# Performance work log

Hardware: AMD Instinct MI355X
Metric: run time of the kernel (lower is better)

The kernel has to match this reference:

```python
import jax, jax.numpy as jnp
import numpy as np

NUM_MODES = 192
LAYERS = [NUM_MODES * 2, 256, 128, 32]


def setup_inputs() -> dict:
    key = jax.random.key(0)
    ks = jax.random.split(key, 7)
    B, C, L = 64, 512, 1024
    x = jax.random.normal(ks[0], (B, C, L), dtype=jnp.float32)
    params = {}
    for i in range(3):
        fan_in, fan_out = LAYERS[i], LAYERS[i + 1]
        bound = 1.0 / np.sqrt(fan_in)
        params[f"W{i+1}"] = jax.random.uniform(ks[1 + 2 * i], (fan_in, fan_out), dtype=jnp.float32, minval=-bound, maxval=bound)
        params[f"b{i+1}"] = jax.random.uniform(ks[2 + 2 * i], (fan_out,), dtype=jnp.float32, minval=-bound, maxval=bound)
    return {"x": x, **params}


def reference(x, W1, b1, W2, b2, W3, b3):
    # rfft over last dim -> complex [B, C, L//2+1]
    f = jnp.fft.rfft(x, axis=-1)
    # view_as_real + slice first NUM_MODES bins -> [B, C, NUM_MODES, 2] (real, imag interleaved)
    f = f[..., :NUM_MODES]
    feat = jnp.stack([f.real, f.imag], axis=-1).reshape(*x.shape[:-1], NUM_MODES * 2)
    h = jax.nn.leaky_relu(feat @ W1 + b1, negative_slope=0.01)
    h = jax.nn.leaky_relu(h @ W2 + b2, negative_slope=0.01)
    return h @ W3 + b3
```

## Files before the change

### kernel.cpp

```cpp
#include <hip/hip_runtime.h>
#include <hip/hip_bf16.h>

typedef __attribute__((ext_vector_type(8))) short short8;
typedef __attribute__((ext_vector_type(4))) float f32x4;

__device__ __forceinline__ short8 load_af(const unsigned short* p) {
  union { uint2 u[2]; short8 v; } r;
  r.u[0] = *(const uint2*)(p);
  r.u[1] = *(const uint2*)(p + 16);
  return r.v;
}

__device__ __forceinline__ unsigned int pk_bf16(float a, float b) {
  __hip_bfloat162 h = __float22bfloat162_rn(make_float2(a, b));
  return *(unsigned int*)&h;
}
__device__ __forceinline__ unsigned short s_bf16(float a) {
  __hip_bfloat16 h = __float2bfloat16(a);
  return *(unsigned short*)&h;
}

__device__ __forceinline__ short8 cvt_af(const float4& lo, const float4& hi) {
  union { uint4 u; short8 v; } r;
  r.u.x = pk_bf16(lo.x, lo.y);
  r.u.y = pk_bf16(lo.z, lo.w);
  r.u.z = pk_bf16(hi.x, hi.y);
  r.u.w = pk_bf16(hi.z, hi.w);
  return r.v;
}

__global__ __launch_bounds__(256) void prep_kernel(
    const float* __restrict__ W1, const float* __restrict__ W2,
    const float* __restrict__ W3,
    unsigned short* __restrict__ fL1, unsigned short* __restrict__ fL2,
    unsigned short* __restrict__ fL3) {
  const int w = blockIdx.x * 4 + (threadIdx.x >> 6);
  const int lane = threadIdx.x & 63;
  const int rlo = lane & 15;
  const int q4 = (lane >> 4) << 2;

  if (w < 512) {
    const int nt = w >> 5, kk = w & 31;
    const int col = nt * 16 + rlo;
    const int k0 = kk * 32 + q4;
    float pc[8], ps[8], dc[8], dsn[8], acc[8];
#pragma unroll
    for (int e = 0; e < 8; ++e) {
      int ke = k0 + (e & 3) + ((e >> 2) << 4);
      float ang = (float)ke * 6.135923151542565e-3f;
      float s, c;
      __sincosf(ang, &s, &c);
      dc[e] = c; dsn[e] = s;
      pc[e] = 1.f; ps[e] = 0.f;
      acc[e] = 0.f;
    }
    const float* pw = W1 + col;
#pragma unroll 2
    for (int m = 0; m < 192; ++m) {
      float wre = pw[0];
      float wio = pw[256];
      pw += 512;
#pragma unroll
      for (int e = 0; e < 8; ++e) {
        acc[e] = fmaf(pc[e], wre, acc[e]);
        acc[e] = fmaf(-ps[e], wio, acc[e]);
        float c2 = pc[e] * dc[e] - ps[e] * dsn[e];
        float s2 = ps[e] * dc[e] + pc[e] * dsn[e];
        pc[e] = c2; ps[e] = s2;
      }
    }
    uint4 v;
    v.x = pk_bf16(acc[0], acc[1]);
    v.y = pk_bf16(acc[2], acc[3]);
    v.z = pk_bf16(acc[4], acc[5]);
    v.w = pk_bf16(acc[6], acc[7]);
    *(uint4*)(fL1 + ((size_t)w * 64 + lane) * 8) = v;
  } else if (w < 576) {
    const int tl = w - 512;
    const int nt = tl >> 3, kk = tl & 7;
    const int col = nt * 16 + rlo;
    const int k0 = kk * 32 + q4;
    float a[8];
#pragma unroll
    for (int e = 0; e < 8; ++e) {
      int ke = k0 + (e & 3) + ((e >> 2) << 4);
      a[e] = W2[ke * 128 + col];
    }
    uint4 v;
    v.x = pk_bf16(a[0], a[1]); v.y = pk_bf16(a[2], a[3]);
    v.z = pk_bf16(a[4], a[5]); v.w = pk_bf16(a[6], a[7]);
    *(uint4*)(fL2 + ((size_t)tl * 64 + lane) * 8) = v;
  } else {
    const int tl = w - 576;
    const int nt = tl >> 2, kk = tl & 3;
    const int col = nt * 16 + rlo;
    const int k0 = kk * 32 + q4;
    float a[8];
#pragma unroll
    for (int e = 0; e < 8; ++e) {
      int ke = k0 + (e & 3) + ((e >> 2) << 4);
      a[e] = W3[ke * 32 + col];
    }
    uint4 v;
    v.x = pk_bf16(a[0], a[1]); v.y = pk_bf16(a[2], a[3]);
    v.z = pk_bf16(a[4], a[5]); v.w = pk_bf16(a[6], a[7]);
    *(uint4*)(fL3 + ((size_t)tl * 64 + lane) * 8) = v;
  }
}

#define H1_S 260
#define H2_S 132

__global__ __launch_bounds__(256, 2) void mlp_kernel(
    const float* __restrict__ x,
    const float* __restrict__ b1, const float* __restrict__ b2,
    const float* __restrict__ b3,
    const unsigned short* __restrict__ fL1, const unsigned short* __restrict__ fL2,
    const unsigned short* __restrict__ fL3, float* __restrict__ out) {
  __shared__ unsigned short h1s[64 * H1_S];
  __shared__ unsigned short h2s[64 * H2_S];
  const int t = threadIdx.x;
  const int lane = t & 63;
  const int wid = t >> 6;
  const int rlo = lane & 15;
  const int g4 = (lane >> 4) << 2;
  const size_t row0 = (size_t)blockIdx.x * 64;

  const float* xb = x + (row0 + rlo) * 1024 + g4;
  const unsigned short* fb = fL1 + ((size_t)wid * 4 * 32 * 64 + lane) * 8;

  f32x4 acc[4][4] = {};

  float4 ac[4][2], an[4][2];
  short8 bc[4], bn[4];
#pragma unroll
  for (int m = 0; m < 4; ++m) {
    ac[m][0] = *(const float4*)(xb + m * 16384);
    ac[m][1] = *(const float4*)(xb + m * 16384 + 16);
  }
#pragma unroll
  for (int c = 0; c < 4; ++c)
    bc[c] = *(const short8*)(fb + (size_t)c * 32 * 512);

#pragma unroll 2
  for (int kk = 0; kk < 32; ++kk) {
    if (kk < 31) {
#pragma unroll
      for (int m = 0; m < 4; ++m) {
        an[m][0] = *(const float4*)(xb + m * 16384 + (kk + 1) * 32);
        an[m][1] = *(const float4*)(xb + m * 16384 + (kk + 1) * 32 + 16);
      }
#pragma unroll
      for (int c = 0; c < 4; ++c)
        bn[c] = *(const short8*)(fb + ((size_t)c * 32 + kk + 1) * 512);
    }
    short8 af[4];
#pragma unroll
    for (int m = 0; m < 4; ++m) af[m] = cvt_af(ac[m][0], ac[m][1]);
#pragma unroll
    for (int m = 0; m < 4; ++m)
#pragma unroll
      for (int c = 0; c < 4; ++c)
        acc[m][c] = __builtin_amdgcn_mfma_f32_16x16x32_bf16(af[m], bc[c], acc[m][c], 0, 0, 0);
    if (kk < 31) {
#pragma unroll
      for (int m = 0; m < 4; ++m) { ac[m][0] = an[m][0]; ac[m][1] = an[m][1]; }
#pragma unroll
      for (int c = 0; c < 4; ++c) bc[c] = bn[c];
    }
  }

  {
    float bv[4];
#pragma unroll
    for (int c = 0; c < 4; ++c) bv[c] = b1[wid * 64 + c * 16 + rlo];
#pragma unroll
    for (int m = 0; m < 4; ++m)
#pragma unroll
      for (int c = 0; c < 4; ++c)
#pragma unroll
        for (int r = 0; r < 4; ++r) {
          float v = acc[m][c][r] + bv[c];
          v = fmaxf(v, 0.01f * v);
          h1s[(m * 16 + g4 + r) * H1_S + wid * 64 + c * 16 + rlo] = s_bf16(v);
        }
  }
  __syncthreads();

  f32x4 a2[4][2] = {};
#pragma unroll
  for (int ks = 0; ks < 8; ++ks) {
    short8 af[4];
#pragma unroll
    for (int m = 0; m < 4; ++m)
      af[m] = load_af(h1s + (m * 16 + rlo) * H1_S + ks * 32 + g4);
    short8 bfr[2];
#pragma unroll
    for (int c = 0; c < 2; ++c)
      bfr[c] = *(const short8*)(fL2 + (((size_t)(wid * 2 + c) * 8 + ks) * 64 + lane) * 8);
#pragma unroll
    for (int m = 0; m < 4; ++m)
#pragma unroll
      for (int c = 0; c < 2; ++c)
        a2[m][c] = __builtin_amdgcn_mfma_f32_16x16x32_bf16(af[m], bfr[c], a2[m][c], 0, 0, 0);
  }
  {
    float bv[2];
#pragma unroll
    for (int c = 0; c < 2; ++c) bv[c] = b2[wid * 32 + c * 16 + rlo];
#pragma unroll
    for (int m = 0; m < 4; ++m)
#pragma unroll
      for (int c = 0; c < 2; ++c)
#pragma unroll
        for (int r = 0; r < 4; ++r) {
          float v = a2[m][c][r] + bv[c];
          v = fmaxf(v, 0.01f * v);
          h2s[(m * 16 + g4 + r) * H2_S + wid * 32 + c * 16 + rlo] = s_bf16(v);
        }
  }
  __syncthreads();

  f32x4 a3[2] = {};
#pragma unroll
  for (int ks = 0; ks < 4; ++ks) {
    short8 af = load_af(h2s + (wid * 16 + rlo) * H2_S + ks * 32 + g4);
#pragma unroll
    for (int c = 0; c < 2; ++c) {
      short8 bfr = *(const short8*)(fL3 + (((size_t)c * 4 + ks) * 64 + lane) * 8);
      a3[c] = __builtin_amdgcn_mfma_f32_16x16x32_bf16(af, bfr, a3[c], 0, 0, 0);
    }
  }
  {
    float bv[2];
    bv[0] = b3[rlo];
    bv[1] = b3[16 + rlo];
#pragma unroll
    for (int c = 0; c < 2; ++c)
#pragma unroll
      for (int r = 0; r < 4; ++r)
        out[(row0 + wid * 16 + g4 + r) * 32 + c * 16 + rlo] = a3[c][r] + bv[c];
  }
}

extern "C" void kernel_launch(void* const* d_in, const int* in_sizes, int n_in,
                              void* d_out, int out_size, void* d_ws, size_t ws_size,
                              hipStream_t stream) {
  const float* x  = (const float*)d_in[0];
  const float* W1 = (const float*)d_in[1];
  const float* b1 = (const float*)d_in[2];
  const float* W2 = (const float*)d_in[3];
  const float* b2 = (const float*)d_in[4];
  const float* W3 = (const float*)d_in[5];
  const float* b3 = (const float*)d_in[6];
  float* out = (float*)d_out;

  char* ws = (char*)d_ws;
  unsigned short* fL1 = (unsigned short*)ws;
  unsigned short* fL2 = (unsigned short*)(ws + 524288);
  unsigned short* fL3 = (unsigned short*)(ws + 589824);

  hipLaunchKernelGGL(prep_kernel, dim3(146), dim3(256), 0, stream,
                     W1, W2, W3, fL1, fL2, fL3);
  hipLaunchKernelGGL(mlp_kernel, dim3(512), dim3(256), 0, stream,
                     x, b1, b2, b3, fL1, fL2, fL3, out);
}
```

Before: 291.9 us.

## Split fused MLP into separate layer-1 GEMM and layers-2/3 kernels with smaller tiles

Splits the fused kernel in two. The first kernel does the DFT-folded first GEMM on 32-row tiles and writes bf16 activations to a global workspace. The second kernel reads them back, with register double-buffering, for layers 2 and 3. Halving the row tile doubles the number of blocks and raises the occupancy hint, to improve latency hiding and CU utilisation. The cost is an extra global round trip for h1 (about 16MB of bf16 writes plus reads), an extra launch, and twice the reloading of the W1 fragments across blocks.

```diff
diff --git a/kernel.cpp b/kernel.cpp
--- a/kernel.cpp
+++ b/kernel.cpp
@@ -3,13 +3,6 @@
 
 typedef __attribute__((ext_vector_type(8))) short short8;
 typedef __attribute__((ext_vector_type(4))) float f32x4;
-
-__device__ __forceinline__ short8 load_af(const unsigned short* p) {
-  union { uint2 u[2]; short8 v; } r;
-  r.u[0] = *(const uint2*)(p);
-  r.u[1] = *(const uint2*)(p + 16);
-  return r.v;
-}
 
 __device__ __forceinline__ unsigned int pk_bf16(float a, float b) {
   __hip_bfloat162 h = __float22bfloat162_rn(make_float2(a, b));
@@ -26,6 +19,12 @@
   r.u.y = pk_bf16(lo.z, lo.w);
   r.u.z = pk_bf16(hi.x, hi.y);
   r.u.w = pk_bf16(hi.z, hi.w);
+  return r.v;
+}
+
+__device__ __forceinline__ short8 mk_af(uint2 a, uint2 b) {
+  union { uint2 u[2]; short8 v; } r;
+  r.u[0] = a; r.u[1] = b;
   return r.v;
 }
 
@@ -108,33 +107,26 @@
   }
 }
 
-#define H1_S 260
-#define H2_S 132
-
-__global__ __launch_bounds__(256, 2) void mlp_kernel(
-    const float* __restrict__ x,
-    const float* __restrict__ b1, const float* __restrict__ b2,
-    const float* __restrict__ b3,
-    const unsigned short* __restrict__ fL1, const unsigned short* __restrict__ fL2,
-    const unsigned short* __restrict__ fL3, float* __restrict__ out) {
-  __shared__ unsigned short h1s[64 * H1_S];
-  __shared__ unsigned short h2s[64 * H2_S];
+__global__ __launch_bounds__(256, 4) void gemm1_kernel(
+    const float* __restrict__ x, const float* __restrict__ b1,
+    const unsigned short* __restrict__ fL1,
+    unsigned short* __restrict__ h1g) {
   const int t = threadIdx.x;
   const int lane = t & 63;
   const int wid = t >> 6;
   const int rlo = lane & 15;
   const int g4 = (lane >> 4) << 2;
-  const size_t row0 = (size_t)blockIdx.x * 64;
+  const size_t row0 = (size_t)blockIdx.x * 32;
 
   const float* xb = x + (row0 + rlo) * 1024 + g4;
-  const unsigned short* fb = fL1 + ((size_t)wid * 4 * 32 * 64 + lane) * 8;
-
-  f32x4 acc[4][4] = {};
-
-  float4 ac[4][2], an[4][2];
+  const unsigned short* fb = fL1 + ((size_t)wid * 4 * 32 * 512) + (size_t)lane * 8;
+
+  f32x4 acc[2][4] = {};
+  float4 ac[2][2], an[2][2];
   short8 bc[4], bn[4];
-#pragma unroll
-  for (int m = 0; m < 4; ++m) {
+
+#pragma unroll
+  for (int m = 0; m < 2; ++m) {
     ac[m][0] = *(const float4*)(xb + m * 16384);
     ac[m][1] = *(const float4*)(xb + m * 16384 + 16);
   }
@@ -146,7 +138,7 @@
   for (int kk = 0; kk < 32; ++kk) {
     if (kk < 31) {
 #pragma unroll
-      for (int m = 0; m < 4; ++m) {
+      for (int m = 0; m < 2; ++m) {
         an[m][0] = *(const float4*)(xb + m * 16384 + (kk + 1) * 32);
         an[m][1] = *(const float4*)(xb + m * 16384 + (kk + 1) * 32 + 16);
       }
@@ -154,84 +146,122 @@
       for (int c = 0; c < 4; ++c)
         bn[c] = *(const short8*)(fb + ((size_t)c * 32 + kk + 1) * 512);
     }
-    short8 af[4];
-#pragma unroll
-    for (int m = 0; m < 4; ++m) af[m] = cvt_af(ac[m][0], ac[m][1]);
-#pragma unroll
-    for (int m = 0; m < 4; ++m)
+    short8 af[2];
+#pragma unroll
+    for (int m = 0; m < 2; ++m) af[m] = cvt_af(ac[m][0], ac[m][1]);
+#pragma unroll
+    for (int m = 0; m < 2; ++m)
 #pragma unroll
       for (int c = 0; c < 4; ++c)
         acc[m][c] = __builtin_amdgcn_mfma_f32_16x16x32_bf16(af[m], bc[c], acc[m][c], 0, 0, 0);
     if (kk < 31) {
 #pragma unroll
-      for (int m = 0; m < 4; ++m) { ac[m][0] = an[m][0]; ac[m][1] = an[m][1]; }
+      for (int m = 0; m < 2; ++m) { ac[m][0] = an[m][0]; ac[m][1] = an[m][1]; }
 #pragma unroll
       for (int c = 0; c < 4; ++c) bc[c] = bn[c];
     }
   }
 
-  {
-    float bv[4];
-#pragma unroll
-    for (int c = 0; c < 4; ++c) bv[c] = b1[wid * 64 + c * 16 + rlo];
-#pragma unroll
-    for (int m = 0; m < 4; ++m)
-#pragma unroll
-      for (int c = 0; c < 4; ++c)
-#pragma unroll
-        for (int r = 0; r < 4; ++r) {
-          float v = acc[m][c][r] + bv[c];
-          v = fmaxf(v, 0.01f * v);
-          h1s[(m * 16 + g4 + r) * H1_S + wid * 64 + c * 16 + rlo] = s_bf16(v);
-        }
-  }
-  __syncthreads();
-
-  f32x4 a2[4][2] = {};
+  float bv[4];
+#pragma unroll
+  for (int c = 0; c < 4; ++c) bv[c] = b1[wid * 64 + c * 16 + rlo];
+#pragma unroll
+  for (int m = 0; m < 2; ++m)
+#pragma unroll
+    for (int c = 0; c < 4; ++c)
+#pragma unroll
+      for (int r = 0; r < 4; ++r) {
+        float v = acc[m][c][r] + bv[c];
+        v = fmaxf(v, 0.01f * v);
+        h1g[(row0 + m * 16 + g4 + r) * 256 + wid * 64 + c * 16 + rlo] = s_bf16(v);
+      }
+}
+
+#define H2S 132
+
+__global__ __launch_bounds__(256, 4) void mlp2_kernel(
+    const unsigned short* __restrict__ h1g,
+    const float* __restrict__ b2, const float* __restrict__ b3,
+    const unsigned short* __restrict__ fL2, const unsigned short* __restrict__ fL3,
+    float* __restrict__ out) {
+  __shared__ unsigned short h2s[32 * H2S];
+  const int t = threadIdx.x;
+  const int lane = t & 63;
+  const int wid = t >> 6;
+  const int rlo = lane & 15;
+  const int g4 = (lane >> 4) << 2;
+  const size_t row0 = (size_t)blockIdx.x * 32;
+
+  const unsigned short* hb = h1g + (row0 + rlo) * 256 + g4;
+
+  f32x4 a2[2][2] = {};
+  uint2 acu[2][2], anx[2][2];
+  short8 b2c[2], b2n[2];
+#pragma unroll
+  for (int m = 0; m < 2; ++m) {
+    acu[m][0] = *(const uint2*)(hb + m * 4096);
+    acu[m][1] = *(const uint2*)(hb + m * 4096 + 16);
+  }
+#pragma unroll
+  for (int c = 0; c < 2; ++c)
+    b2c[c] = *(const short8*)(fL2 + (((size_t)(wid * 2 + c) * 8) * 64 + lane) * 8);
+
 #pragma unroll
   for (int ks = 0; ks < 8; ++ks) {
-    short8 af[4];
-#pragma unroll
-    for (int m = 0; m < 4; ++m)
-      af[m] = load_af(h1s + (m * 16 + rlo) * H1_S + ks * 32 + g4);
-    short8 bfr[2];
-#pragma unroll
-    for (int c = 0; c < 2; ++c)
-      bfr[c] = *(const short8*)(fL2 + (((size_t)(wid * 2 + c) * 8 + ks) * 64 + lane) * 8);
-#pragma unroll
-    for (int m = 0; m < 4; ++m)
+    if (ks < 7) {
+#pragma unroll
+      for (int m = 0; m < 2; ++m) {
+        anx[m][0] = *(const uint2*)(hb + m * 4096 + (ks + 1) * 32);
+        anx[m][1] = *(const uint2*)(hb + m * 4096 + (ks + 1) * 32 + 16);
+      }
 #pragma unroll
       for (int c = 0; c < 2; ++c)
-        a2[m][c] = __builtin_amdgcn_mfma_f32_16x16x32_bf16(af[m], bfr[c], a2[m][c], 0, 0, 0);
+        b2n[c] = *(const short8*)(fL2 + (((size_t)(wid * 2 + c) * 8 + ks + 1) * 64 + lane) * 8);
+    }
+    short8 af[2];
+#pragma unroll
+    for (int m = 0; m < 2; ++m) af[m] = mk_af(acu[m][0], acu[m][1]);
+#pragma unroll
+    for (int m = 0; m < 2; ++m)
+#pragma unroll
+      for (int c = 0; c < 2; ++c)
+        a2[m][c] = __builtin_amdgcn_mfma_f32_16x16x32_bf16(af[m], b2c[c], a2[m][c], 0, 0, 0);
+    if (ks < 7) {
+#pragma unroll
+      for (int m = 0; m < 2; ++m) { acu[m][0] = anx[m][0]; acu[m][1] = anx[m][1]; }
+#pragma unroll
+      for (int c = 0; c < 2; ++c) b2c[c] = b2n[c];
+    }
   }
   {
     float bv[2];
 #pragma unroll
     for (int c = 0; c < 2; ++c) bv[c] = b2[wid * 32 + c * 16 + rlo];
 #pragma unroll
-    for (int m = 0; m < 4; ++m)
+    for (int m = 0; m < 2; ++m)
 #pragma unroll
       for (int c = 0; c < 2; ++c)
 #pragma unroll
         for (int r = 0; r < 4; ++r) {
           float v = a2[m][c][r] + bv[c];
           v = fmaxf(v, 0.01f * v);
-          h2s[(m * 16 + g4 + r) * H2_S + wid * 32 + c * 16 + rlo] = s_bf16(v);
+          h2s[(m * 16 + g4 + r) * H2S + wid * 32 + c * 16 + rlo] = s_bf16(v);
         }
   }
   __syncthreads();
 
-  f32x4 a3[2] = {};
-#pragma unroll
-  for (int ks = 0; ks < 4; ++ks) {
-    short8 af = load_af(h2s + (wid * 16 + rlo) * H2_S + ks * 32 + g4);
-#pragma unroll
-    for (int c = 0; c < 2; ++c) {
-      short8 bfr = *(const short8*)(fL3 + (((size_t)c * 4 + ks) * 64 + lane) * 8);
-      a3[c] = __builtin_amdgcn_mfma_f32_16x16x32_bf16(af, bfr, a3[c], 0, 0, 0);
-    }
-  }
-  {
+  if (wid < 2) {
+    f32x4 a3[2] = {};
+#pragma unroll
+    for (int ks = 0; ks < 4; ++ks) {
+      const unsigned short* p = h2s + (wid * 16 + rlo) * H2S + ks * 32 + g4;
+      short8 af = mk_af(*(const uint2*)p, *(const uint2*)(p + 16));
+#pragma unroll
+      for (int c = 0; c < 2; ++c) {
+        short8 bfr = *(const short8*)(fL3 + (((size_t)c * 4 + ks) * 64 + lane) * 8);
+        a3[c] = __builtin_amdgcn_mfma_f32_16x16x32_bf16(af, bfr, a3[c], 0, 0, 0);
+      }
+    }
     float bv[2];
     bv[0] = b3[rlo];
     bv[1] = b3[16 + rlo];
@@ -259,9 +289,12 @@
   unsigned short* fL1 = (unsigned short*)ws;
   unsigned short* fL2 = (unsigned short*)(ws + 524288);
   unsigned short* fL3 = (unsigned short*)(ws + 589824);
+  unsigned short* h1g = (unsigned short*)(ws + 1048576);
 
   hipLaunchKernelGGL(prep_kernel, dim3(146), dim3(256), 0, stream,
                      W1, W2, W3, fL1, fL2, fL3);
-  hipLaunchKernelGGL(mlp_kernel, dim3(512), dim3(256), 0, stream,
-                     x, b1, b2, b3, fL1, fL2, fL3, out);
-}
+  hipLaunchKernelGGL(gemm1_kernel, dim3(1024), dim3(256), 0, stream,
+                     x, b1, fL1, h1g);
+  hipLaunchKernelGGL(mlp2_kernel, dim3(1024), dim3(256), 0, stream,
+                     h1g, b2, b3, fL2, fL3, out);
+}
```

Result: slower. 330.4 us (+13.2%).
